# Kernel optimization log

Measured on AMD Instinct MI355X. Metric: run time of the kernel, lower is better.

## Reference

```python
import jax, jax.numpy as jnp
import numpy as np
import math

DIM = 384
NH = 6
DH = DIM // NH
B = 2
S = 2048
EPS = 1e-6
LN_EPS = 1e-5


def setup_inputs() -> dict:
    key = jax.random.key(0)
    ks = jax.random.split(key, 8)
    q = jax.random.normal(ks[0], (B, S, DIM), dtype=jnp.float32)
    k = jax.random.normal(ks[1], (B, S, DIM), dtype=jnp.float32)
    v = jax.random.normal(ks[2], (B, S, DIM), dtype=jnp.float32)
    # gate linear params (Linear(3*dim, num_heads)); small random weights to exercise the math
    igate_w = jax.random.normal(ks[3], (NH, 3 * DIM), dtype=jnp.float32) * 0.02
    igate_b = jax.random.normal(ks[4], (NH,), dtype=jnp.float32) * 0.1
    fgate_w = jax.random.normal(ks[5], (NH, 3 * DIM), dtype=jnp.float32) * 0.02
    fgate_b = jnp.linspace(3.0, 6.0, NH, dtype=jnp.float32)
    # MultiHeadLayerNorm residual weight (stored as delta, effective scale = 1 + w)
    outnorm_weight = jax.random.normal(ks[6], (DIM,), dtype=jnp.float32) * 0.02
    return {"q": q, "k": k, "v": v, "igate_w": igate_w, "igate_b": igate_b,
            "fgate_w": fgate_w, "fgate_b": fgate_b, "outnorm_weight": outnorm_weight}


def _mlstm_forward(q, k, v, igate_w, igate_b, fgate_w, fgate_b, outnorm_weight):
    Bq, Sq, _ = q.shape
    gate_in = jnp.concatenate([q, k, v], axis=-1)                       # (B,S,3D)
    ig = gate_in @ igate_w.T + igate_b                                   # (B,S,NH)
    fg = gate_in @ fgate_w.T + fgate_b                                   # (B,S,NH)
    # split heads: (B,NH,S,DH)
    qh = q.reshape(Bq, Sq, NH, DH).transpose(0, 2, 1, 3)
    kh = k.reshape(Bq, Sq, NH, DH).transpose(0, 2, 1, 3)
    vh = v.reshape(Bq, Sq, NH, DH).transpose(0, 2, 1, 3)
    ig = ig.transpose(0, 2, 1)                                           # (B,NH,S)
    fg = fg.transpose(0, 2, 1)                                           # (B,NH,S)

    log_fg = jax.nn.log_sigmoid(fg)                                      # (B,NH,S)
    lfc = jnp.concatenate([jnp.zeros((Bq, NH, 1), dtype=q.dtype),
                           jnp.cumsum(log_fg, axis=-1)], axis=-1)        # (B,NH,S+1)
    # log_fg_matrix[i,j] = cumsum[i] - cumsum[j] (sliced [1:,1:]), masked causal
    diff = lfc[:, :, 1:, None] - lfc[:, :, None, 1:]                     # (B,NH,S,S)
    ltr = jnp.tril(jnp.ones((Sq, Sq), dtype=bool))
    log_fg_mat = jnp.where(ltr, diff, -jnp.inf)
    log_D = log_fg_mat + ig[:, :, None, :]                               # + igate^T
    max_log_D = jnp.max(log_D, axis=-1, keepdims=True)                   # rowwise stabilize
    D = jnp.exp(log_D - max_log_D)
    qk = jnp.einsum('bhsd,bhtd->bhst', qh, kh) / math.sqrt(DH)
    C = qk * D
    normalizer = jnp.maximum(jnp.abs(jnp.sum(C, axis=-1, keepdims=True)),
                             jnp.exp(-max_log_D))
    h = jnp.einsum('bhst,bhtd->bhsd', C / (normalizer + EPS), vh)        # (B,NH,S,DH)

    # MultiHeadLayerNorm == group_norm over each head's DH channels, scale=(1+w)
    mean = jnp.mean(h, axis=-1, keepdims=True)
    var = jnp.var(h, axis=-1, keepdims=True)
    normed = (h - mean) / jnp.sqrt(var + LN_EPS)
    scale = (1.0 + outnorm_weight).reshape(NH, DH)[None, :, None, :]
    out = normed * scale
    return out.transpose(0, 2, 1, 3).reshape(Bq, Sq, DIM)


def reference(q, k, v, igate_w, igate_b, fgate_w, fgate_b, outnorm_weight):
    return _mlstm_forward(q, k, v, igate_w, igate_b, fgate_w, fgate_b, outnorm_weight)
```

## Files before the change

kernel.cpp:

```cpp
#include <hip/hip_runtime.h>
#include <math.h>

#define DIM 384
#define NH 6
#define DH 64
#define B_ 2
#define S_ 2048
#define EPS 1e-6f
#define LN_EPS 1e-5f
#define G3 (3*DIM)
#define LOG2E 1.44269504f
#define KSTR 72
#define NT (S_/64)
#define NSPLIT 4
#define NBH (B_*NH)

typedef __attribute__((ext_vector_type(8))) short bf16x8;
typedef __attribute__((ext_vector_type(4))) short bf16x4;
typedef __attribute__((ext_vector_type(4))) float f32x4;
typedef __attribute__((ext_vector_type(8))) unsigned short u16x8;

__device__ __forceinline__ unsigned short f2bf(float f){
    unsigned int u = __float_as_uint(f);
    u += 0x7fff + ((u >> 16) & 1);
    return (unsigned short)(u >> 16);
}
__device__ __forceinline__ float bf2f(unsigned short u){
    return __uint_as_float(((unsigned int)u) << 16);
}
__device__ __forceinline__ float logsig(float x){
    return fminf(x, 0.f) - log1pf(expf(-fabsf(x)));
}

__global__ __launch_bounds__(256) void cvtqk_kernel(
    const float* __restrict__ q, const float* __restrict__ k,
    unsigned short* __restrict__ Qb, unsigned short* __restrict__ Kb) {
    size_t base = ((size_t)blockIdx.x * 256 + threadIdx.x) * 8;
    float4 a = *(const float4*)(q + base);
    float4 b = *(const float4*)(q + base + 4);
    u16x8 t;
    t[0]=f2bf(a.x*0.125f); t[1]=f2bf(a.y*0.125f); t[2]=f2bf(a.z*0.125f); t[3]=f2bf(a.w*0.125f);
    t[4]=f2bf(b.x*0.125f); t[5]=f2bf(b.y*0.125f); t[6]=f2bf(b.z*0.125f); t[7]=f2bf(b.w*0.125f);
    *(u16x8*)(Qb + base) = t;
    float4 c = *(const float4*)(k + base);
    float4 d = *(const float4*)(k + base + 4);
    u16x8 s;
    s[0]=f2bf(c.x); s[1]=f2bf(c.y); s[2]=f2bf(c.z); s[3]=f2bf(c.w);
    s[4]=f2bf(d.x); s[5]=f2bf(d.y); s[6]=f2bf(d.z); s[7]=f2bf(d.w);
    *(u16x8*)(Kb + base) = s;
}

__global__ __launch_bounds__(256) void cvtv_kernel(
    const float* __restrict__ v, unsigned short* __restrict__ Vt) {
    __shared__ unsigned short lt[64*KSTR];
    int bh = blockIdx.y;
    int b = bh / NH, h = bh % NH;
    int t0 = blockIdx.x * 64;
    int tid = threadIdx.x;
    #pragma unroll
    for (int i = 0; i < 4; i++){
        int idx = tid + 256*i;
        int r = idx >> 4;
        int c4 = (idx & 15) * 4;
        float4 x = *(const float4*)(v + ((size_t)b*S_ + t0 + r)*DIM + h*DH + c4);
        lt[(c4+0)*KSTR + r] = f2bf(x.x);
        lt[(c4+1)*KSTR + r] = f2bf(x.y);
        lt[(c4+2)*KSTR + r] = f2bf(x.z);
        lt[(c4+3)*KSTR + r] = f2bf(x.w);
    }
    __syncthreads();
    #pragma unroll
    for (int i = 0; i < 2; i++){
        int idx = tid + 256*i;
        int d = idx >> 3;
        int t8 = (idx & 7) * 8;
        u16x8 o = *(const u16x8*)&lt[d*KSTR + t8];
        *(u16x8*)(Vt + (size_t)bh*DH*S_ + (size_t)d*S_ + t0 + t8) = o;
    }
}

__global__ __launch_bounds__(256) void gates_kernel(
    const float* __restrict__ q, const float* __restrict__ k, const float* __restrict__ v,
    const float* __restrict__ iw, const float* __restrict__ ib,
    const float* __restrict__ fw, const float* __restrict__ fb,
    float* __restrict__ ig_out, float* __restrict__ lf_out) {
    int wave = (blockIdx.x * 256 + threadIdx.x) >> 6;
    int lane = threadIdx.x & 63;
    int b = wave / S_, s = wave % S_;
    size_t base = ((size_t)b * S_ + s) * DIM;
    float aI[NH], aF[NH];
    #pragma unroll
    for (int h = 0; h < NH; h++){ aI[h] = 0.f; aF[h] = 0.f; }
    for (int g = lane; g < G3/4; g += 64) {
        int e = g * 4;
        float4 x4;
        if (e < DIM)        x4 = *(const float4*)(q + base + e);
        else if (e < 2*DIM) x4 = *(const float4*)(k + base + e - DIM);
        else                x4 = *(const float4*)(v + base + e - 2*DIM);
        #pragma unroll
        for (int h = 0; h < NH; h++){
            float4 wi = *(const float4*)(iw + h*G3 + e);
            float4 wf = *(const float4*)(fw + h*G3 + e);
            aI[h] = fmaf(x4.x, wi.x, fmaf(x4.y, wi.y, fmaf(x4.z, wi.z, fmaf(x4.w, wi.w, aI[h]))));
            aF[h] = fmaf(x4.x, wf.x, fmaf(x4.y, wf.y, fmaf(x4.z, wf.z, fmaf(x4.w, wf.w, aF[h]))));
        }
    }
    #pragma unroll
    for (int h = 0; h < NH; h++){
        #pragma unroll
        for (int off = 32; off >= 1; off >>= 1){
            aI[h] += __shfl_xor(aI[h], off, 64);
            aF[h] += __shfl_xor(aF[h], off, 64);
        }
    }
    if (lane == 0) {
        #pragma unroll
        for (int h = 0; h < NH; h++){
            ig_out[((size_t)b*NH + h)*S_ + s] = aI[h] + ib[h];
            lf_out[((size_t)b*NH + h)*S_ + s] = logsig(aF[h] + fb[h]);
        }
    }
}

__global__ __launch_bounds__(256) void scan_kernel(const float* __restrict__ lf,
                                                   float* __restrict__ cum){
    int bh = blockIdx.x;
    const float* src = lf + (size_t)bh * S_;
    float* dst = cum + (size_t)bh * S_;
    int tid = threadIdx.x;
    float loc[8];
    float run = 0.f;
    #pragma unroll
    for (int j = 0; j < 8; j++){ run += src[tid*8 + j]; loc[j] = run; }
    __shared__ float sm[256];
    sm[tid] = run;
    __syncthreads();
    float total = run;
    for (int off = 1; off < 256; off <<= 1){
        float vv = (tid >= off) ? sm[tid - off] : 0.f;
        __syncthreads();
        sm[tid] += vv;
        __syncthreads();
    }
    float excl = sm[tid] - total;
    #pragma unroll
    for (int j = 0; j < 8; j++) dst[tid*8 + j] = excl + loc[j];
}

__global__ __launch_bounds__(256) void mlstm_part(
    const unsigned short* __restrict__ Qb, const unsigned short* __restrict__ Kb,
    const unsigned short* __restrict__ Vt,
    const float* __restrict__ ig, const float* __restrict__ cum,
    unsigned short* __restrict__ pOb, float* __restrict__ pM, float* __restrict__ pL) {
    int lin = blockIdx.x;
    int sp  = lin / NBH;
    int bh  = lin % NBH;
    int st  = (NT - 1) - (sp >> 2);
    int c   = sp & 3;
    int L   = (st + 4) >> 2;
    int tb0 = c * L;
    int tb1 = min((c + 1) * L, st + 1);
    int pblk = lin;
    int tid = threadIdx.x;

    if (tb0 >= tb1){
        if (tid < 64){ pM[pblk*64 + tid] = -INFINITY; pL[pblk*64 + tid] = 0.f; }
        return;
    }

    __shared__ unsigned short kt[64*KSTR];
    __shared__ unsigned short vt[64*KSTR];

    int b = bh / NH, h = bh % NH;
    int s0 = st * 64;
    int wv   = tid >> 6;
    int lane = tid & 63;
    int lq   = lane & 15;
    int quad = lane >> 4;

    const unsigned short* kbT = Kb + (size_t)b*S_*DIM + h*DH;
    const unsigned short* vtB = Vt + (size_t)bh*DH*S_;
    const float* igb = ig + (size_t)bh*S_;
    const float* cmb = cum + (size_t)bh*S_;

    int s_glob = s0 + 16*wv + lq;

    bf16x8 qf[2];
    {
        const unsigned short* qr = Qb + ((size_t)b*S_ + s_glob)*DIM + h*DH;
        qf[0] = *(const bf16x8*)(qr + 8*quad);
        qf[1] = *(const bf16x8*)(qr + 32 + 8*quad);
    }

    float cq  = cmb[s_glob];
    float m_s = -INFINITY, b_s = 0.f;
    f32x4 oacc[4];
    #pragma unroll
    for (int cg = 0; cg < 4; cg++) oacc[cg] = (f32x4){0.f,0.f,0.f,0.f};

    int sr[2], sc[2];
    #pragma unroll
    for (int i = 0; i < 2; i++){
        int idx = tid + 256*i;
        sr[i] = idx >> 3;
        sc[i] = (idx & 7) * 8;
    }

    u16x8 kreg[2], vreg[2];
    {
        const unsigned short* kb = kbT + (size_t)(tb0*64)*DIM;
        const unsigned short* vb = vtB + tb0*64;
        #pragma unroll
        for (int i = 0; i < 2; i++){
            kreg[i] = *(const u16x8*)(kb + (size_t)sr[i]*DIM + sc[i]);
            vreg[i] = *(const u16x8*)(vb + (size_t)sr[i]*S_ + sc[i]);
        }
    }

    for (int t0 = tb0*64; t0 < tb1*64; t0 += 64){
        float4 cumc[4], igc[4];
        #pragma unroll
        for (int tb = 0; tb < 4; tb++){
            cumc[tb] = *(const float4*)(cmb + t0 + 16*tb + 4*quad);
            igc[tb]  = *(const float4*)(igb + t0 + 16*tb + 4*quad);
        }

        __syncthreads();
        #pragma unroll
        for (int i = 0; i < 2; i++){
            *(u16x8*)&kt[sr[i]*KSTR + sc[i]] = kreg[i];
            *(u16x8*)&vt[sr[i]*KSTR + sc[i]] = vreg[i];
        }
        __syncthreads();

        if (t0 + 64 < tb1*64){
            const unsigned short* kb = kbT + (size_t)(t0 + 64)*DIM;
            const unsigned short* vb = vtB + (t0 + 64);
            #pragma unroll
            for (int i = 0; i < 2; i++){
                kreg[i] = *(const u16x8*)(kb + (size_t)sr[i]*DIM + sc[i]);
                vreg[i] = *(const u16x8*)(vb + (size_t)sr[i]*S_ + sc[i]);
            }
        }

        f32x4 st4[4];
        #pragma unroll
        for (int tb = 0; tb < 4; tb++) st4[tb] = (f32x4){0.f,0.f,0.f,0.f};
        #pragma unroll
        for (int ks = 0; ks < 2; ks++){
            #pragma unroll
            for (int tb = 0; tb < 4; tb++){
                bf16x8 af = *(const bf16x8*)&kt[(16*tb + lq)*KSTR + 32*ks + 8*quad];
                st4[tb] = __builtin_amdgcn_mfma_f32_16x16x32_bf16(af, qf[ks], st4[tb], 0, 0, 0);
            }
        }

        bool diag = (t0 == s0);
        float dv[4][4];
        float pmax = -INFINITY;
        #pragma unroll
        for (int tb = 0; tb < 4; tb++){
            #pragma unroll
            for (int r = 0; r < 4; r++){
                float d = cq - cumc[tb][r] + igc[tb][r];
                if (diag && (t0 + 16*tb + 4*quad + r) > s_glob) d = -INFINITY;
                dv[tb][r] = d;
                pmax = fmaxf(pmax, d);
            }
        }
        pmax = fmaxf(pmax, __shfl_xor(pmax, 16, 64));
        pmax = fmaxf(pmax, __shfl_xor(pmax, 32, 64));
        float mn = fmaxf(m_s, pmax);
        float sc2 = exp2f((m_s - mn) * LOG2E);
        m_s = mn;
        float rs = 0.f;
        bf16x4 pf[4];
        #pragma unroll
        for (int tb = 0; tb < 4; tb++){
            #pragma unroll
            for (int r = 0; r < 4; r++){
                float pv = st4[tb][r] * exp2f((dv[tb][r] - mn) * LOG2E);
                rs += pv;
                pf[tb][r] = (short)f2bf(pv);
            }
        }
        rs += __shfl_xor(rs, 16, 64);
        rs += __shfl_xor(rs, 32, 64);
        b_s = b_s * sc2 + rs;

        #pragma unroll
        for (int r = 0; r < 4; r++){
            float sco = __shfl(sc2, 20*quad + r, 64);
            #pragma unroll
            for (int cg = 0; cg < 4; cg++) oacc[cg][r] *= sco;
        }

        #pragma unroll
        for (int tb = 0; tb < 4; tb++){
            #pragma unroll
            for (int cg = 0; cg < 4; cg++){
                bf16x4 vf = *(const bf16x4*)&vt[(16*cg + lq)*KSTR + 16*tb + 4*quad];
                oacc[cg] = __builtin_amdgcn_mfma_f32_16x16x16bf16_1k(pf[tb], vf, oacc[cg], 0, 0, 0);
            }
        }
    }

    unsigned short* po = pOb + (size_t)pblk * 4096;
    #pragma unroll
    for (int r = 0; r < 4; r++){
        int row = 16*wv + 4*quad + r;
        #pragma unroll
        for (int cg = 0; cg < 4; cg++)
            po[row*64 + 16*cg + lq] = f2bf(oacc[cg][r]);
    }
    if (quad == 0){
        pM[pblk*64 + 16*wv + lq] = m_s;
        pL[pblk*64 + 16*wv + lq] = b_s;
    }
}

__global__ __launch_bounds__(256) void mlstm_combine(
    const unsigned short* __restrict__ pOb, const float* __restrict__ pM,
    const float* __restrict__ pL, const float* __restrict__ w,
    float* __restrict__ out) {
    int st = blockIdx.x;
    int bh = blockIdx.y;
    int b = bh / NH, h = bh % NH;
    int tid = threadIdx.x;
    int cl = (tid & 15) * 4;
    int rb = tid >> 4;

    int pblk[NSPLIT];
    #pragma unroll
    for (int p = 0; p < NSPLIT; p++)
        pblk[p] = (((NT - 1 - st) << 2) + p) * NBH + bh;

    float4 wv4 = *(const float4*)(w + h*DH + cl);

    #pragma unroll
    for (int pass = 0; pass < 4; pass++){
        int row = pass*16 + rb;
        float mp[NSPLIT], lp[NSPLIT];
        float mmax = -INFINITY;
        #pragma unroll
        for (int p = 0; p < NSPLIT; p++){
            mp[p] = pM[pblk[p]*64 + row];
            lp[p] = pL[pblk[p]*64 + row];
            mmax = fmaxf(mmax, mp[p]);
        }
        float l = 0.f;
        float ox = 0.f, oy = 0.f, oz = 0.f, ow = 0.f;
        #pragma unroll
        for (int p = 0; p < NSPLIT; p++){
            if (mp[p] != -INFINITY){
                float wp = exp2f((mp[p] - mmax) * LOG2E);
                l += wp * lp[p];
                ushort4 t4 = *(const ushort4*)(pOb + (size_t)pblk[p]*4096 + row*64 + cl);
                ox += wp*bf2f(t4.x); oy += wp*bf2f(t4.y);
                oz += wp*bf2f(t4.z); ow += wp*bf2f(t4.w);
            }
        }
        float nrm = fmaxf(fabsf(l), exp2f(-mmax * LOG2E));
        float inv = 1.f / (nrm + EPS);
        float x[4] = {ox*inv, oy*inv, oz*inv, ow*inv};
        float s1 = x[0]+x[1]+x[2]+x[3];
        float s2 = x[0]*x[0]+x[1]*x[1]+x[2]*x[2]+x[3]*x[3];
        #pragma unroll
        for (int off = 8; off >= 1; off >>= 1){
            s1 += __shfl_xor(s1, off, 64);
            s2 += __shfl_xor(s2, off, 64);
        }
        float mean = s1 * (1.f/64.f);
        float var  = s2 * (1.f/64.f) - mean*mean;
        float rstd = rsqrtf(var + LN_EPS);
        float4 oo;
        oo.x = (x[0]-mean)*rstd*(1.f + wv4.x);
        oo.y = (x[1]-mean)*rstd*(1.f + wv4.y);
        oo.z = (x[2]-mean)*rstd*(1.f + wv4.z);
        oo.w = (x[3]-mean)*rstd*(1.f + wv4.w);
        *(float4*)(out + ((size_t)b*S_ + st*64 + row)*DIM + h*DH + cl) = oo;
    }
}

extern "C" void kernel_launch(void* const* d_in, const int* in_sizes, int n_in,
                              void* d_out, int out_size, void* d_ws, size_t ws_size,
                              hipStream_t stream) {
    const float* q  = (const float*)d_in[0];
    const float* k  = (const float*)d_in[1];
    const float* v  = (const float*)d_in[2];
    const float* iw = (const float*)d_in[3];
    const float* ib = (const float*)d_in[4];
    const float* fw = (const float*)d_in[5];
    const float* fb = (const float*)d_in[6];
    const float* w  = (const float*)d_in[7];
    float* out = (float*)d_out;

    const int nPart = NBH * NT * NSPLIT;
    const size_t NE = (size_t)B_ * S_ * DIM;
    float* ig  = (float*)d_ws;
    float* lf  = ig  + (size_t)NBH*S_;
    float* cum = lf  + (size_t)NBH*S_;
    float* pM  = cum + (size_t)NBH*S_;
    float* pL  = pM  + (size_t)nPart*64;
    unsigned short* pOb = (unsigned short*)(pL + (size_t)nPart*64);
    unsigned short* Qb  = pOb + (size_t)nPart*4096;
    unsigned short* Kb  = Qb + NE;
    unsigned short* Vt  = Kb + NE;

    cvtqk_kernel<<<NE/8/256, 256, 0, stream>>>(q, k, Qb, Kb);
    cvtv_kernel<<<dim3(NT, NBH), 256, 0, stream>>>(v, Vt);
    gates_kernel<<<B_*S_/4, 256, 0, stream>>>(q, k, v, iw, ib, fw, fb, ig, lf);
    scan_kernel<<<NBH, 256, 0, stream>>>(lf, cum);
    mlstm_part<<<nPart, 256, 0, stream>>>(Qb, Kb, Vt, ig, cum, pOb, pM, pL);
    mlstm_combine<<<dim3(NT, NBH), 256, 0, stream>>>(pOb, pM, pL, w, out);
}
```

Measured before the change: 142.0 us.

## Factor decay matrix into per-row and per-column exponentials, merge conversion kernels

The scan kernel now precomputes, per 64-key tile, exponentials of (igate - cumsum + tile base) along with tile-level and prefix running maxima. The attention loop can then form each weight as a product of one per-row scale and a precomputed per-column factor, which removes the per-element exp2 and the cross-lane max reductions. The q/k/v bf16 conversion kernels are fused into a single launch. The risk is numerical: per-tile factoring relative to a base may overflow or underflow when decay varies strongly within a tile.

```diff
diff --git a/kernel.cpp b/kernel.cpp
--- a/kernel.cpp
+++ b/kernel.cpp
@@ -32,26 +32,10 @@
     return fminf(x, 0.f) - log1pf(expf(-fabsf(x)));
 }
 
-__global__ __launch_bounds__(256) void cvtqk_kernel(
-    const float* __restrict__ q, const float* __restrict__ k,
-    unsigned short* __restrict__ Qb, unsigned short* __restrict__ Kb) {
-    size_t base = ((size_t)blockIdx.x * 256 + threadIdx.x) * 8;
-    float4 a = *(const float4*)(q + base);
-    float4 b = *(const float4*)(q + base + 4);
-    u16x8 t;
-    t[0]=f2bf(a.x*0.125f); t[1]=f2bf(a.y*0.125f); t[2]=f2bf(a.z*0.125f); t[3]=f2bf(a.w*0.125f);
-    t[4]=f2bf(b.x*0.125f); t[5]=f2bf(b.y*0.125f); t[6]=f2bf(b.z*0.125f); t[7]=f2bf(b.w*0.125f);
-    *(u16x8*)(Qb + base) = t;
-    float4 c = *(const float4*)(k + base);
-    float4 d = *(const float4*)(k + base + 4);
-    u16x8 s;
-    s[0]=f2bf(c.x); s[1]=f2bf(c.y); s[2]=f2bf(c.z); s[3]=f2bf(c.w);
-    s[4]=f2bf(d.x); s[5]=f2bf(d.y); s[6]=f2bf(d.z); s[7]=f2bf(d.w);
-    *(u16x8*)(Kb + base) = s;
-}
-
-__global__ __launch_bounds__(256) void cvtv_kernel(
-    const float* __restrict__ v, unsigned short* __restrict__ Vt) {
+__global__ __launch_bounds__(256) void cvt_kernel(
+    const float* __restrict__ q, const float* __restrict__ k, const float* __restrict__ v,
+    unsigned short* __restrict__ Qb, unsigned short* __restrict__ Kb,
+    unsigned short* __restrict__ Vt) {
     __shared__ unsigned short lt[64*KSTR];
     int bh = blockIdx.y;
     int b = bh / NH, h = bh % NH;
@@ -62,11 +46,19 @@
         int idx = tid + 256*i;
         int r = idx >> 4;
         int c4 = (idx & 15) * 4;
-        float4 x = *(const float4*)(v + ((size_t)b*S_ + t0 + r)*DIM + h*DH + c4);
-        lt[(c4+0)*KSTR + r] = f2bf(x.x);
-        lt[(c4+1)*KSTR + r] = f2bf(x.y);
-        lt[(c4+2)*KSTR + r] = f2bf(x.z);
-        lt[(c4+3)*KSTR + r] = f2bf(x.w);
+        size_t off = ((size_t)b*S_ + t0 + r)*DIM + h*DH + c4;
+        float4 xq = *(const float4*)(q + off);
+        ushort4 tq; tq.x=f2bf(xq.x*0.125f); tq.y=f2bf(xq.y*0.125f);
+        tq.z=f2bf(xq.z*0.125f); tq.w=f2bf(xq.w*0.125f);
+        *(ushort4*)(Qb + off) = tq;
+        float4 xk = *(const float4*)(k + off);
+        ushort4 tk; tk.x=f2bf(xk.x); tk.y=f2bf(xk.y); tk.z=f2bf(xk.z); tk.w=f2bf(xk.w);
+        *(ushort4*)(Kb + off) = tk;
+        float4 xv = *(const float4*)(v + off);
+        lt[(c4+0)*KSTR + r] = f2bf(xv.x);
+        lt[(c4+1)*KSTR + r] = f2bf(xv.y);
+        lt[(c4+2)*KSTR + r] = f2bf(xv.z);
+        lt[(c4+3)*KSTR + r] = f2bf(xv.w);
     }
     __syncthreads();
     #pragma unroll
@@ -122,16 +114,21 @@
     }
 }
 
-__global__ __launch_bounds__(256) void scan_kernel(const float* __restrict__ lf,
-                                                   float* __restrict__ cum){
+__global__ __launch_bounds__(256) void scan_kernel(
+    const float* __restrict__ lf, const float* __restrict__ ig,
+    float* __restrict__ cum, float* __restrict__ e2, float* __restrict__ pm,
+    float* __restrict__ me, float* __restrict__ baseA){
     int bh = blockIdx.x;
-    const float* src = lf + (size_t)bh * S_;
-    float* dst = cum + (size_t)bh * S_;
+    const float* srcL = lf + (size_t)bh * S_;
+    const float* srcI = ig + (size_t)bh * S_;
+    float* dstC = cum + (size_t)bh * S_;
+    float* dstE = e2 + (size_t)bh * S_;
+    float* dstP = pm + (size_t)bh * S_;
     int tid = threadIdx.x;
     float loc[8];
     float run = 0.f;
     #pragma unroll
-    for (int j = 0; j < 8; j++){ run += src[tid*8 + j]; loc[j] = run; }
+    for (int j = 0; j < 8; j++){ run += srcL[tid*8 + j]; loc[j] = run; }
     __shared__ float sm[256];
     sm[tid] = run;
     __syncthreads();
@@ -143,14 +140,42 @@
         __syncthreads();
     }
     float excl = sm[tid] - total;
-    #pragma unroll
-    for (int j = 0; j < 8; j++) dst[tid*8 + j] = excl + loc[j];
+    float c[8];
+    #pragma unroll
+    for (int j = 0; j < 8; j++){ c[j] = excl + loc[j]; dstC[tid*8 + j] = c[j]; }
+    __shared__ float sb[32];
+    if ((tid & 7) == 0) sb[tid >> 3] = excl;
+    __syncthreads();
+    float base_t = sb[tid >> 3];
+    float E[8], mloc = -INFINITY;
+    #pragma unroll
+    for (int j = 0; j < 8; j++){
+        E[j] = srcI[tid*8 + j] - c[j] + base_t;
+        dstE[tid*8 + j] = exp2f(E[j] * LOG2E);
+        mloc = fmaxf(mloc, E[j]);
+    }
+    __shared__ float smax[256];
+    smax[tid] = mloc;
+    __syncthreads();
+    float carry = -INFINITY;
+    int g0 = tid & ~7;
+    for (int u = g0; u < tid; u++) carry = fmaxf(carry, smax[u]);
+    float runm = carry;
+    #pragma unroll
+    for (int j = 0; j < 8; j++){
+        runm = fmaxf(runm, E[j]);
+        dstP[tid*8 + j] = runm;
+    }
+    if ((tid & 7) == 7) me[bh*NT + (tid >> 3)] = runm;
+    if ((tid & 7) == 0) baseA[bh*NT + (tid >> 3)] = base_t;
 }
 
 __global__ __launch_bounds__(256) void mlstm_part(
     const unsigned short* __restrict__ Qb, const unsigned short* __restrict__ Kb,
     const unsigned short* __restrict__ Vt,
-    const float* __restrict__ ig, const float* __restrict__ cum,
+    const float* __restrict__ cum, const float* __restrict__ e2,
+    const float* __restrict__ pm, const float* __restrict__ me,
+    const float* __restrict__ baseA,
     unsigned short* __restrict__ pOb, float* __restrict__ pM, float* __restrict__ pL) {
     int lin = blockIdx.x;
     int sp  = lin / NBH;
@@ -180,8 +205,10 @@
 
     const unsigned short* kbT = Kb + (size_t)b*S_*DIM + h*DH;
     const unsigned short* vtB = Vt + (size_t)bh*DH*S_;
-    const float* igb = ig + (size_t)bh*S_;
     const float* cmb = cum + (size_t)bh*S_;
+    const float* e2b = e2 + (size_t)bh*S_;
+    const float* meB = me + bh*NT;
+    const float* baseB = baseA + bh*NT;
 
     int s_glob = s0 + 16*wv + lq;
 
@@ -192,7 +219,8 @@
         qf[1] = *(const bf16x8*)(qr + 32 + 8*quad);
     }
 
-    float cq  = cmb[s_glob];
+    float cq   = cmb[s_glob];
+    float pm_s = pm[(size_t)bh*S_ + s_glob];
     float m_s = -INFINITY, b_s = 0.f;
     f32x4 oacc[4];
     #pragma unroll
@@ -218,12 +246,13 @@
     }
 
     for (int t0 = tb0*64; t0 < tb1*64; t0 += 64){
-        float4 cumc[4], igc[4];
-        #pragma unroll
-        for (int tb = 0; tb < 4; tb++){
-            cumc[tb] = *(const float4*)(cmb + t0 + 16*tb + 4*quad);
-            igc[tb]  = *(const float4*)(igb + t0 + 16*tb + 4*quad);
-        }
+        int tix = t0 >> 6;
+        float base_t = baseB[tix];
+        float me_t   = meB[tix];
+        float4 e2v[4];
+        #pragma unroll
+        for (int tb = 0; tb < 4; tb++)
+            e2v[tb] = *(const float4*)(e2b + t0 + 16*tb + 4*quad);
 
         __syncthreads();
         #pragma unroll
@@ -256,32 +285,35 @@
         }
 
         bool diag = (t0 == s0);
-        float dv[4][4];
-        float pmax = -INFINITY;
-        #pragma unroll
-        for (int tb = 0; tb < 4; tb++){
-            #pragma unroll
-            for (int r = 0; r < 4; r++){
-                float d = cq - cumc[tb][r] + igc[tb][r];
-                if (diag && (t0 + 16*tb + 4*quad + r) > s_glob) d = -INFINITY;
-                dv[tb][r] = d;
-                pmax = fmaxf(pmax, d);
-            }
-        }
-        pmax = fmaxf(pmax, __shfl_xor(pmax, 16, 64));
-        pmax = fmaxf(pmax, __shfl_xor(pmax, 32, 64));
+        float A = cq - base_t;
+        float pmax = A + (diag ? pm_s : me_t);
         float mn = fmaxf(m_s, pmax);
         float sc2 = exp2f((m_s - mn) * LOG2E);
+        float ws = exp2f((A - mn) * LOG2E);
         m_s = mn;
+        float pv[4][4];
+        #pragma unroll
+        for (int tb = 0; tb < 4; tb++){
+            #pragma unroll
+            for (int r = 0; r < 4; r++)
+                pv[tb][r] = st4[tb][r] * (ws * e2v[tb][r]);
+        }
+        if (diag){
+            #pragma unroll
+            for (int tb = 0; tb < 4; tb++){
+                #pragma unroll
+                for (int r = 0; r < 4; r++)
+                    if (t0 + 16*tb + 4*quad + r > s_glob) pv[tb][r] = 0.f;
+            }
+        }
         float rs = 0.f;
         bf16x4 pf[4];
         #pragma unroll
         for (int tb = 0; tb < 4; tb++){
             #pragma unroll
             for (int r = 0; r < 4; r++){
-                float pv = st4[tb][r] * exp2f((dv[tb][r] - mn) * LOG2E);
-                rs += pv;
-                pf[tb][r] = (short)f2bf(pv);
+                rs += pv[tb][r];
+                pf[tb][r] = (short)f2bf(pv[tb][r]);
             }
         }
         rs += __shfl_xor(rs, 16, 64);
@@ -397,20 +429,23 @@
 
     const int nPart = NBH * NT * NSPLIT;
     const size_t NE = (size_t)B_ * S_ * DIM;
-    float* ig  = (float*)d_ws;
-    float* lf  = ig  + (size_t)NBH*S_;
-    float* cum = lf  + (size_t)NBH*S_;
-    float* pM  = cum + (size_t)NBH*S_;
-    float* pL  = pM  + (size_t)nPart*64;
+    float* ig   = (float*)d_ws;
+    float* lf   = ig   + (size_t)NBH*S_;
+    float* cum  = lf   + (size_t)NBH*S_;
+    float* e2   = cum  + (size_t)NBH*S_;
+    float* pm   = e2   + (size_t)NBH*S_;
+    float* me   = pm   + (size_t)NBH*S_;
+    float* base = me   + (size_t)NBH*NT;
+    float* pM   = base + (size_t)NBH*NT;
+    float* pL   = pM   + (size_t)nPart*64;
     unsigned short* pOb = (unsigned short*)(pL + (size_t)nPart*64);
     unsigned short* Qb  = pOb + (size_t)nPart*4096;
     unsigned short* Kb  = Qb + NE;
     unsigned short* Vt  = Kb + NE;
 
-    cvtqk_kernel<<<NE/8/256, 256, 0, stream>>>(q, k, Qb, Kb);
-    cvtv_kernel<<<dim3(NT, NBH), 256, 0, stream>>>(v, Vt);
+    cvt_kernel<<<dim3(NT, NBH), 256, 0, stream>>>(q, k, v, Qb, Kb, Vt);
     gates_kernel<<<B_*S_/4, 256, 0, stream>>>(q, k, v, iw, ib, fw, fb, ig, lf);
-    scan_kernel<<<NBH, 256, 0, stream>>>(lf, cum);
-    mlstm_part<<<nPart, 256, 0, stream>>>(Qb, Kb, Vt, ig, cum, pOb, pM, pL);
+    scan_kernel<<<NBH, 256, 0, stream>>>(lf, ig, cum, e2, pm, me, base);
+    mlstm_part<<<nPart, 256, 0, stream>>>(Qb, Kb, Vt, cum, e2, pm, me, base, pOb, pM, pL);
     mlstm_combine<<<dim3(NT, NBH), 256, 0, stream>>>(pOb, pM, pL, w, out);
 }
```

Result: faster. 134.1 us (-5.6%).
